# Optimization experiments

Hardware: AMD Instinct MI355X
Metric: run time of the kernel (lower is better)

The kernel has to match this reference:

```python
import jax, jax.numpy as jnp
import numpy as np

B, L, C, D, H, NB, K = 8, 1024, 4, 64, 8, 2, 16  # batch, seq, conds, dim, heads, blocks, rbf centers

def _ln(x, s, b):
    m = x.mean(-1, keepdims=True)
    v = x.var(-1, keepdims=True)
    return (x - m) / jnp.sqrt(v + 1e-6) * s + b

def setup_inputs() -> dict:
    key = jax.random.key(0)
    ks = jax.random.split(key, 24)
    rn = lambda i, shape, sc=0.02: jax.random.normal(ks[i], shape, jnp.float32) * sc
    inp = {}
    inp['z'] = jax.random.normal(ks[0], (B, L), jnp.float32)
    inp['conditionals'] = jax.random.normal(ks[1], (C,), jnp.float32)
    inp['s'] = jnp.sort(jax.random.uniform(ks[2], (L,), jnp.float32))
    inp['embed'] = rn(3, (L, 2 * D - (C + 1)))  # positional id embedding table
    # input MLP([4D, D]) with gelu
    inp['Win1'] = rn(4, (2 * D, 4 * D)); inp['bin1'] = jnp.zeros((4 * D,), jnp.float32)
    inp['Win2'] = rn(5, (4 * D, D));     inp['bin2'] = jnp.zeros((D,), jnp.float32)
    # per-block (leading dim NB) transformer params
    inp['ln1_s'] = jnp.ones((NB, D), jnp.float32); inp['ln1_b'] = jnp.zeros((NB, D), jnp.float32)
    inp['ln2_s'] = jnp.ones((NB, D), jnp.float32); inp['ln2_b'] = jnp.zeros((NB, D), jnp.float32)
    inp['Wq'] = rn(6, (NB, D, 2 * D)); inp['bq'] = jnp.zeros((NB, 2 * D), jnp.float32)
    inp['Wk'] = rn(7, (NB, D, 2 * D)); inp['bk'] = jnp.zeros((NB, 2 * D), jnp.float32)
    inp['Wv'] = rn(8, (NB, D, 2 * D)); inp['bv'] = jnp.zeros((NB, 2 * D), jnp.float32)
    inp['Wo'] = rn(9, (NB, 2 * D, D)); inp['bo'] = jnp.zeros((NB, D), jnp.float32)
    # RBF-network attention bias: features exp(-(d-c)^2/(2w^2)) -> linear to H heads
    inp['rbf_c'] = jnp.tile(jnp.linspace(-1.0, 1.0, K, dtype=jnp.float32)[None], (NB, 1))
    inp['rbf_logw'] = jnp.full((NB, K), -1.0, jnp.float32)
    inp['rbf_w'] = rn(10, (NB, K, H), 0.1); inp['rbf_b'] = jnp.zeros((NB, H), jnp.float32)
    # FFN MLP([4D, D])
    inp['W1'] = rn(11, (NB, D, 4 * D)); inp['b1'] = jnp.zeros((NB, 4 * D), jnp.float32)
    inp['W2'] = rn(12, (NB, 4 * D, D)); inp['b2'] = jnp.zeros((NB, D), jnp.float32)
    # head MLP([4D, D, 1])
    inp['Wh1'] = rn(13, (D, 4 * D)); inp['bh1'] = jnp.zeros((4 * D,), jnp.float32)
    inp['Wh2'] = rn(14, (4 * D, D)); inp['bh2'] = jnp.zeros((D,), jnp.float32)
    inp['Wh3'] = rn(15, (D, 1));     inp['bh3'] = jnp.zeros((1,), jnp.float32)
    return inp

def reference(z, conditionals, s, embed, Win1, bin1, Win2, bin2,
              ln1_s, ln1_b, ln2_s, ln2_b, Wq, bq, Wk, bk, Wv, bv, Wo, bo,
              rbf_c, rbf_logw, rbf_w, rbf_b, W1, b1, W2, b2,
              Wh1, bh1, Wh2, bh2, Wh3, bh3):
    Bn, Ln = z.shape
    Cn = conditionals.shape[0]
    Hn = rbf_w.shape[-1]
    dh = Wq.shape[-1] // Hn
    scale = 1.0 / jnp.sqrt(jnp.float32(dh))
    # cond_as_feats: [z, broadcast conditionals] -> (B, L, C+1); prepend ids embedding -> (B, L, 2D)
    feats = jnp.concatenate([
        jnp.broadcast_to(embed[None], (Bn,) + embed.shape),
        z[..., None],
        jnp.broadcast_to(conditionals[None, None, :], (Bn, Ln, Cn)),
    ], axis=-1)
    x = jax.nn.gelu(feats @ Win1 + bin1) @ Win2 + bin2  # (B, L, D)
    dist = s[:, None] - s[None, :]  # (L, L) pairwise query-key coordinate diff (same per batch)
    for i in range(Wq.shape[0]):
        h = _ln(x, ln1_s[i], ln1_b[i])
        q = (h @ Wq[i] + bq[i]).reshape(Bn, Ln, Hn, dh)
        k = (h @ Wk[i] + bk[i]).reshape(Bn, Ln, Hn, dh)
        v = (h @ Wv[i] + bv[i]).reshape(Bn, Ln, Hn, dh)
        scores = jnp.einsum('bqhd,bkhd->bhqk', q, k) * scale
        # RBF-network bias on pairwise distances, per head
        phi = jnp.exp(-(dist[..., None] - rbf_c[i]) ** 2 / (2.0 * jnp.exp(rbf_logw[i]) ** 2))  # (L, L, K)
        bias = jnp.einsum('qkf,fh->hqk', phi, rbf_w[i]) + rbf_b[i][:, None, None]  # (H, L, L)
        a = jax.nn.softmax(scores + bias[None], axis=-1)
        o = jnp.einsum('bhqk,bkhd->bqhd', a, v).reshape(Bn, Ln, Hn * dh)
        x = x + o @ Wo[i] + bo[i]
        h2 = _ln(x, ln2_s[i], ln2_b[i])
        x = x + jax.nn.gelu(h2 @ W1[i] + b1[i]) @ W2[i] + b2[i]
    hh = jax.nn.gelu(x @ Wh1 + bh1)
    hh = jax.nn.gelu(hh @ Wh2 + bh2)
    return hh @ Wh3 + bh3  # f_hat: (B, L, 1)
```

## Files before the change

### kernel.cpp

```cpp
#include <hip/hip_runtime.h>
#include <hip/hip_bf16.h>

#define BB   8
#define LL   1024
#define DD   64
#define D2   128
#define D4   256
#define HH   8
#define DH   16

typedef __attribute__((ext_vector_type(8))) short short8;
typedef __attribute__((ext_vector_type(4))) float floatx4;

#define LOG2E 1.4426950408889634f
#define QK_SEED -66.54214054f

#define OB_HALF 1048576
#define L_HALF  65536

#define OFF_WIN1   0
#define OFF_WIN2   65536
#define OFF_LAY0   98304
#define LAY_STRIDE 131072
#define OFF_WQ     0
#define OFF_WK     16384
#define OFF_WV     32768
#define OFF_WO     49152
#define OFF_W1     65536
#define OFF_W2     98304
#define OFF_WH1    360448
#define OFF_WH2    393216

__device__ __forceinline__ float gelu_tanh(float u) {
  float t = tanhf(0.7978845608028654f * (u + 0.044715f * u * u * u));
  return 0.5f * u * (1.0f + t);
}

__device__ __forceinline__ float wave_reduce_sum(float v) {
#pragma unroll
  for (int m = 32; m >= 1; m >>= 1) v += __shfl_xor(v, m, 64);
  return v;
}

__device__ __forceinline__ unsigned short f2bf(float x) {
  unsigned u = __float_as_uint(x);
  u += 0x7fffu + ((u >> 16) & 1u);
  return (unsigned short)(u >> 16);
}

__device__ __forceinline__ float bf2f(unsigned short x) {
  return __uint_as_float(((unsigned)x) << 16);
}

__device__ __forceinline__ void split_bf(float v, unsigned short& hi,
                                         unsigned short& lo) {
  hi = f2bf(v);
  lo = f2bf(v - bf2f(hi));
}

__device__ __forceinline__ unsigned pack_bf2(float a, float b) {
  unsigned ua = __float_as_uint(a) + 0x8000u;
  unsigned ub = __float_as_uint(b) + 0x8000u;
  return __builtin_amdgcn_perm(ub, ua, 0x07060302u);
}

template <int K, int KP>
__device__ __forceinline__ floatx4 mfma_tile(
    const unsigned short* Ah, const unsigned short* Al,
    const unsigned short* __restrict__ Bh, const unsigned short* __restrict__ Bl,
    int lq, int quad, floatx4 C) {
#pragma unroll
  for (int kk = 0; kk < K; kk += 32) {
    short8 ah = *(const short8*)(Ah + lq * KP + kk + quad * 8);
    short8 al = *(const short8*)(Al + lq * KP + kk + quad * 8);
    short8 bh = *(const short8*)(Bh + lq * K + kk + quad * 8);
    short8 bl = *(const short8*)(Bl + lq * K + kk + quad * 8);
    C = __builtin_amdgcn_mfma_f32_16x16x32_bf16(ah, bh, C, 0, 0, 0);
    C = __builtin_amdgcn_mfma_f32_16x16x32_bf16(al, bh, C, 0, 0, 0);
    C = __builtin_amdgcn_mfma_f32_16x16x32_bf16(ah, bl, C, 0, 0, 0);
  }
  return C;
}

struct PrepArgs {
  const float* src[16];
  int Kd[16], Nd[16], dst[16], elems[16];
};

__global__ __launch_bounds__(256) void k_prep_bias(
    PrepArgs a, unsigned short* __restrict__ arena,
    const float* __restrict__ s, const float* __restrict__ rbf_c,
    const float* __restrict__ rbf_logw, const float* __restrict__ rbf_w,
    const float* __restrict__ rbf_b, unsigned short* __restrict__ biasT) {
  int bid = blockIdx.x, t = threadIdx.x;
  if (bid < 2048) {
    int mid = bid >> 7;
    int e = (bid & 127) * 256 + t;
    int KN = a.elems[mid];
    if (e >= KN) return;
    int K = a.Kd[mid], N = a.Nd[mid];
    int n = e / K, k = e - n * K;
    float wv = a.src[mid][k * N + n];
    unsigned short hi, lo;
    split_bf(wv, hi, lo);
    arena[a.dst[mid] + e] = hi;
    arena[a.dst[mid] + KN + e] = lo;
    return;
  }
  int rem = bid - 2048;
  int lay = rem >> 12;
  int id = (rem & 4095) * 256 + t;
  int q = id >> 10, k = id & 1023;
  float dd = s[q] - s[k];
  float acc[8];
#pragma unroll
  for (int h = 0; h < 8; ++h) acc[h] = rbf_b[lay * 8 + h];
#pragma unroll 1
  for (int f = 0; f < 16; ++f) {
    float c = rbf_c[lay * 16 + f];
    float inv2w2 = 0.5f * __expf(-2.0f * rbf_logw[lay * 16 + f]);
    float e = dd - c;
    float ph = __expf(-e * e * inv2w2);
#pragma unroll
    for (int h = 0; h < 8; ++h)
      acc[h] = fmaf(ph, rbf_w[lay * 128 + f * 8 + h], acc[h]);
  }
  unsigned short* bT = biasT + (size_t)lay * 8 * 1024 * 1024;
#pragma unroll
  for (int h = 0; h < 8; ++h)
    bT[(size_t)(h * 1024 + q) * 1024 + k] = f2bf(acc[h] * LOG2E);
}

__device__ __forceinline__ void qkv_tail(
    const float* xl, unsigned short* Sh, unsigned short* Sl,
    const unsigned short* __restrict__ arena, int lay,
    const float* __restrict__ ln_s, const float* __restrict__ ln_b,
    const float* __restrict__ bq, const float* __restrict__ bk,
    const float* __restrict__ bv, unsigned short* __restrict__ qo,
    unsigned short* __restrict__ ko, unsigned short* __restrict__ voT,
    int tok0, int t) {
  int w = t >> 6, lane = t & 63;
  int lq = lane & 15, quad = lane >> 4;
  float ss = ln_s[lay * 64 + lane], sb = ln_b[lay * 64 + lane];
#pragma unroll
  for (int tk = 0; tk < 4; ++tk) {
    int tok = w * 4 + tk;
    float v = xl[tok * 64 + lane];
    float mean = wave_reduce_sum(v) * 0.015625f;
    float d = v - mean;
    float var = wave_reduce_sum(d * d) * 0.015625f;
    float hv = d * rsqrtf(var + 1e-6f) * ss + sb;
    unsigned short hi, lo;
    split_bf(hv, hi, lo);
    Sh[tok * 72 + lane] = hi;
    Sl[tok * 72 + lane] = lo;
  }
  __syncthreads();
  int b = tok0 >> 10, l0 = tok0 & 1023;
#pragma unroll 1
  for (int mat = 0; mat < 3; ++mat) {
    const unsigned short* Bh =
        arena + OFF_LAY0 + lay * LAY_STRIDE + mat * 16384;
    const unsigned short* Bl = Bh + 8192;
    const float* bias = (mat == 0 ? bq : mat == 1 ? bk : bv) + lay * 128;
#pragma unroll
    for (int j = 0; j < 2; ++j) {
      int tl = w + j * 4;
      int n = tl * 16 + lq;
      float bb = bias[n];
      floatx4 C = {bb, bb, bb, bb};
      C = mfma_tile<64, 72>(Sh, Sl, Bh + tl * 16 * 64, Bl + tl * 16 * 64,
                            lq, quad, C);
      if (mat < 2) {
        unsigned short* outp = (mat == 0 ? qo : ko);
        size_t basea = ((size_t)(b * 8 + tl) * 1024 + l0 + quad * 4) * 16 + lq;
#pragma unroll
        for (int r = 0; r < 4; ++r)
          outp[basea + (size_t)r * 16] = f2bf(C[r]);
      } else {
        size_t basev = ((size_t)(b * 8 + tl) * 16 + lq) * 1024 + l0 + quad * 4;
#pragma unroll
        for (int r = 0; r < 4; ++r)
          voT[basev + r] = f2bf(C[r]);
      }
    }
  }
}

__global__ __launch_bounds__(256) void k_in_qkv(
    const float* __restrict__ embed, const float* __restrict__ z,
    const float* __restrict__ cond, const unsigned short* __restrict__ arena,
    const float* __restrict__ bin1, const float* __restrict__ bin2,
    float* __restrict__ x, const float* __restrict__ ln1_s,
    const float* __restrict__ ln1_b, const float* __restrict__ bq,
    const float* __restrict__ bk, const float* __restrict__ bv,
    unsigned short* __restrict__ qo, unsigned short* __restrict__ ko,
    unsigned short* __restrict__ voT) {
  __shared__ __align__(16) unsigned short Ah[16 * 136], Al[16 * 136];
  __shared__ __align__(16) unsigned short Hh[16 * 264], Hl[16 * 264];
  __shared__ __align__(16) unsigned short Sh[16 * 72], Sl[16 * 72];
  __shared__ float xl[16 * 64];
  int t = threadIdx.x, w = t >> 6, lane = t & 63;
  int lq = lane & 15, quad = lane >> 4;
  int tok0 = blockIdx.x * 16;
  for (int idx = t; idx < 2048; idx += 256) {
    int tok = idx >> 7, dim = idx & 127;
    int bl = tok0 + tok, l = bl & (LL - 1);
    float v;
    if (dim < 123) v = embed[l * 123 + dim];
    else if (dim == 123) v = z[bl];
    else v = cond[dim - 124];
    unsigned short hi, lo;
    split_bf(v, hi, lo);
    Ah[tok * 136 + dim] = hi;
    Al[tok * 136 + dim] = lo;
  }
  __syncthreads();
  const unsigned short* B1h = arena + OFF_WIN1;
  const unsigned short* B1l = B1h + 32768;
#pragma unroll
  for (int j = 0; j < 4; ++j) {
    int tl = w * 4 + j, n = tl * 16 + lq;
    float bb = bin1[n];
    floatx4 C = {bb, bb, bb, bb};
    C = mfma_tile<128, 136>(Ah, Al, B1h + tl * 16 * 128, B1l + tl * 16 * 128,
                            lq, quad, C);
#pragma unroll
    for (int r = 0; r < 4; ++r) {
      float g = gelu_tanh(C[r]);
      unsigned short hi, lo;
      split_bf(g, hi, lo);
      Hh[(quad * 4 + r) * 264 + n] = hi;
      Hl[(quad * 4 + r) * 264 + n] = lo;
    }
  }
  __syncthreads();
  const unsigned short* B2h = arena + OFF_WIN2;
  const unsigned short* B2l = B2h + 16384;
  {
    int n = w * 16 + lq;
    float bb = bin2[n];
    floatx4 C = {bb, bb, bb, bb};
    C = mfma_tile<256, 264>(Hh, Hl, B2h + w * 16 * 256, B2l + w * 16 * 256,
                            lq, quad, C);
#pragma unroll
    for (int r = 0; r < 4; ++r) {
      int m = quad * 4 + r;
      x[(size_t)(tok0 + m) * 64 + n] = C[r];
      xl[m * 64 + n] = C[r];
    }
  }
  __syncthreads();
  qkv_tail(xl, Sh, Sl, arena, 0, ln1_s, ln1_b, bq, bk, bv,
           qo, ko, voT, tok0, t);
}

__global__ __launch_bounds__(256) void k_attn(
    const unsigned short* __restrict__ qg, const unsigned short* __restrict__ kg,
    const unsigned short* __restrict__ vgT, const unsigned short* __restrict__ biasT,
    float* __restrict__ og, float* __restrict__ lsum) {
  __shared__ __align__(16) unsigned short Kl[64 * 32];
  __shared__ __align__(16) unsigned short VT[16 * 72];
  __shared__ __align__(16) unsigned short Pl[4][16 * 72];
  __shared__ __align__(16) unsigned short Bch[64 * 72];
  int t = threadIdx.x, w = t >> 6, lane = t & 63;
  int lq = lane & 15, quad = lane >> 4;
  int bid = blockIdx.x;
  int half = bid >> 10;
  int rem = bid & 1023;
  int b = rem >> 7, h = (rem >> 4) & 7, qblk = rem & 15;
  int q0w = qblk * 64 + w * 16;
  int kbase = half * 512;
  size_t bh = (size_t)(b * 8 + h) * 1024;
  size_t bh16 = (size_t)(b * 8 + h) * 16;

  ((uint4*)Kl)[t] = uint4{0, 0, 0, 0};

  short8 Qb = {};
  if (quad < 2)
    Qb = *(const short8*)(qg + (bh + q0w + lq) * 16 + quad * 8);

  float l = 0.0f;
  floatx4 O = {0.0f, 0.0f, 0.0f, 0.0f};

  int key = t >> 2, dp = (t & 3) * 4;
  int drow = t >> 4, vcol = (t & 15) * 4;
  int qrow = t >> 2, bcol = (t & 3) * 16;
  const unsigned short* kgp = kg + (bh + kbase + key) * 16 + dp;
  const unsigned short* vgp = vgT + (bh16 + drow) * 1024 + kbase + vcol;
  const unsigned short* bgp =
      biasT + ((size_t)(h * 1024 + qblk * 64 + qrow)) * 1024 + kbase + bcol;

  uint2 kpre = *(const uint2*)(kgp);
  uint2 vpre = *(const uint2*)(vgp);
  uint4 bpre0 = *(const uint4*)(bgp);
  uint4 bpre1 = *(const uint4*)(bgp + 8);

#pragma unroll 1
  for (int kc = 0; kc < 512; kc += 64) {
    __syncthreads();
    *(uint2*)(Kl + key * 32 + dp) = kpre;
    *(uint2*)(VT + drow * 72 + vcol) = vpre;
    *(uint4*)(Bch + qrow * 72 + bcol) = bpre0;
    *(uint4*)(Bch + qrow * 72 + bcol + 8) = bpre1;
    __syncthreads();
    if (kc + 64 < 512) {
      kpre = *(const uint2*)(kgp + (size_t)(kc + 64) * 16);
      vpre = *(const uint2*)(vgp + (kc + 64));
      bpre0 = *(const uint4*)(bgp + (kc + 64));
      bpre1 = *(const uint4*)(bgp + (kc + 64) + 8);
    }
    float psum = 0.0f;
    unsigned short* pw = &Pl[w][lq * 72];
#pragma unroll
    for (int tile = 0; tile < 4; ++tile) {
      short8 A = *(const short8*)(Kl + (tile * 16 + lq) * 32 + quad * 8);
      floatx4 c = {QK_SEED, QK_SEED, QK_SEED, QK_SEED};
      c = __builtin_amdgcn_mfma_f32_16x16x32_bf16(A, Qb, c, 0, 0, 0);
      ushort4 bb = *(const ushort4*)(Bch + (w * 16 + lq) * 72 +
                                     tile * 16 + quad * 4);
      float p0 = exp2f(fmaf(c[0], 0.25f * LOG2E, bf2f(bb.x)));
      float p1 = exp2f(fmaf(c[1], 0.25f * LOG2E, bf2f(bb.y)));
      float p2 = exp2f(fmaf(c[2], 0.25f * LOG2E, bf2f(bb.z)));
      float p3 = exp2f(fmaf(c[3], 0.25f * LOG2E, bf2f(bb.w)));
      psum += (p0 + p1) + (p2 + p3);
      uint2 pk;
      pk.x = pack_bf2(p0, p1);
      pk.y = pack_bf2(p2, p3);
      *(uint2*)(pw + tile * 16 + quad * 4) = pk;
    }
    psum += __shfl_xor(psum, 16, 64);
    psum += __shfl_xor(psum, 32, 64);
    l += psum;
    asm volatile("s_waitcnt lgkmcnt(0)" ::: "memory");
#pragma unroll
    for (int i = 0; i < 2; ++i) {
      short8 Pa = *(const short8*)(pw + i * 32 + quad * 8);
      short8 Vb = *(const short8*)(&VT[lq * 72 + i * 32 + quad * 8]);
      O = __builtin_amdgcn_mfma_f32_16x16x32_bf16(Pa, Vb, O, 0, 0, 0);
    }
  }
  float* ogh = og + (size_t)half * OB_HALF;
#pragma unroll
  for (int r = 0; r < 4; ++r)
    ogh[((size_t)(b * 1024 + q0w + quad * 4 + r)) * 128 + h * 16 + lq] = O[r];
  if (quad == 0)
    lsum[(size_t)half * L_HALF + (size_t)(b * 1024 + q0w + lq) * 8 + h] = l;
}

__device__ __forceinline__ void pf_body(
    const float* __restrict__ ob, const float* __restrict__ lsum,
    const unsigned short* __restrict__ arena,
    const float* __restrict__ bo, float* __restrict__ x,
    const float* __restrict__ ln_s, const float* __restrict__ ln_b,
    const float* __restrict__ b1, const float* __restrict__ b2, int lay,
    unsigned short* Ah, unsigned short* Al, unsigned short* Sh,
    unsigned short* Sl, unsigned short* Hh, unsigned short* Hl, float* xl,
    int tok0, int t, bool write_x) {
  int w = t >> 6, lane = t & 63;
  int lq = lane & 15, quad = lane >> 4;
  const unsigned short* labase = arena + OFF_LAY0 + lay * LAY_STRIDE;
  const float* ob1 = ob + OB_HALF;
  for (int idx = t * 4; idx < 2048; idx += 1024) {
    int row = idx >> 7, col = idx & 127;
    int hh = col >> 4;
    int tok = tok0 + row;
    float lv = lsum[(size_t)tok * 8 + hh] +
               lsum[L_HALF + (size_t)tok * 8 + hh];
    float linv = 1.0f / lv;
    float4 v0 = *(const float4*)(ob + (size_t)tok * 128 + col);
    float4 v1 = *(const float4*)(ob1 + (size_t)tok * 128 + col);
    float4 v;
    v.x = (v0.x + v1.x) * linv;
    v.y = (v0.y + v1.y) * linv;
    v.z = (v0.z + v1.z) * linv;
    v.w = (v0.w + v1.w) * linv;
    unsigned short h0, e0, h1, e1, h2, e2, h3, e3;
    split_bf(v.x, h0, e0); split_bf(v.y, h1, e1);
    split_bf(v.z, h2, e2); split_bf(v.w, h3, e3);
    unsigned* ph = (unsigned*)(Ah + row * 136 + col);
    ph[0] = (unsigned)h0 | ((unsigned)h1 << 16);
    ph[1] = (unsigned)h2 | ((unsigned)h3 << 16);
    unsigned* pl = (unsigned*)(Al + row * 136 + col);
    pl[0] = (unsigned)e0 | ((unsigned)e1 << 16);
    pl[1] = (unsigned)e2 | ((unsigned)e3 << 16);
  }
  __syncthreads();
  {
    const unsigned short* Bh = labase + OFF_WO;
    const unsigned short* Bl = Bh + 8192;
    int n = w * 16 + lq;
    float bb = bo[lay * 64 + n];
    floatx4 C = {bb, bb, bb, bb};
    C = mfma_tile<128, 136>(Ah, Al, Bh + w * 16 * 128, Bl + w * 16 * 128,
                            lq, quad, C);
#pragma unroll
    for (int r = 0; r < 4; ++r) {
      int m = quad * 4 + r;
      xl[m * 64 + n] = x[(size_t)(tok0 + m) * 64 + n] + C[r];
    }
  }
  __syncthreads();
  {
    float ss = ln_s[lay * 64 + lane], sb = ln_b[lay * 64 + lane];
#pragma unroll
    for (int tk = 0; tk < 4; ++tk) {
      int tok = w * 4 + tk;
      float v = xl[tok * 64 + lane];
      float mean = wave_reduce_sum(v) * 0.015625f;
      float d = v - mean;
      float var = wave_reduce_sum(d * d) * 0.015625f;
      float hv = d * rsqrtf(var + 1e-6f) * ss + sb;
      unsigned short hi, lo;
      split_bf(hv, hi, lo);
      Sh[tok * 72 + lane] = hi;
      Sl[tok * 72 + lane] = lo;
    }
  }
  __syncthreads();
  {
    const unsigned short* Bh = labase + OFF_W1;
    const unsigned short* Bl = Bh + 16384;
#pragma unroll
    for (int j = 0; j < 4; ++j) {
      int tl = w * 4 + j, n = tl * 16 + lq;
      float bb = b1[lay * 256 + n];
      floatx4 C = {bb, bb, bb, bb};
      C = mfma_tile<64, 72>(Sh, Sl, Bh + tl * 16 * 64, Bl + tl * 16 * 64,
                            lq, quad, C);
#pragma unroll
      for (int r = 0; r < 4; ++r) {
        float g = gelu_tanh(C[r]);
        unsigned short hi, lo;
        split_bf(g, hi, lo);
        Hh[(quad * 4 + r) * 264 + n] = hi;
        Hl[(quad * 4 + r) * 264 + n] = lo;
      }
    }
  }
  __syncthreads();
  {
    const unsigned short* Bh = labase + OFF_W2;
    const unsigned short* Bl = Bh + 16384;
    int n = w * 16 + lq;
    float bb = b2[lay * 64 + n];
    floatx4 C = {bb, bb, bb, bb};
    C = mfma_tile<256, 264>(Hh, Hl, Bh + w * 16 * 256, Bl + w * 16 * 256,
                            lq, quad, C);
#pragma unroll
    for (int r = 0; r < 4; ++r) {
      int m = quad * 4 + r;
      float xv = xl[m * 64 + n] + C[r];
      xl[m * 64 + n] = xv;
      if (write_x) x[(size_t)(tok0 + m) * 64 + n] = xv;
    }
  }
  __syncthreads();
}

__global__ __launch_bounds__(256) void k_pf_qkv(
    const float* __restrict__ ob, const float* __restrict__ lsum,
    const unsigned short* __restrict__ arena,
    const float* __restrict__ bo, float* __restrict__ x,
    const float* __restrict__ ln2_s, const float* __restrict__ ln2_b,
    const float* __restrict__ b1, const float* __restrict__ b2, int lay,
    const float* __restrict__ ln1_s, const float* __restrict__ ln1_b,
    const float* __restrict__ bq, const float* __restrict__ bk,
    const float* __restrict__ bv, unsigned short* __restrict__ qo,
    unsigned short* __restrict__ ko, unsigned short* __restrict__ voT) {
  __shared__ __align__(16) unsigned short Ah[16 * 136], Al[16 * 136];
  __shared__ __align__(16) unsigned short Sh[16 * 72], Sl[16 * 72];
  __shared__ __align__(16) unsigned short Hh[16 * 264], Hl[16 * 264];
  __shared__ float xl[16 * 64];
  int t = threadIdx.x;
  int tok0 = blockIdx.x * 16;
  pf_body(ob, lsum, arena, bo, x, ln2_s, ln2_b, b1, b2, lay,
          Ah, Al, Sh, Sl, Hh, Hl, xl, tok0, t, true);
  qkv_tail(xl, Sh, Sl, arena, lay + 1, ln1_s, ln1_b, bq, bk, bv,
           qo, ko, voT, tok0, t);
}

__global__ __launch_bounds__(256) void k_pf_head(
    const float* __restrict__ ob, const float* __restrict__ lsum,
    const unsigned short* __restrict__ arena,
    const float* __restrict__ bo, float* __restrict__ x,
    const float* __restrict__ ln2_s, const float* __restrict__ ln2_b,
    const float* __restrict__ b1, const float* __restrict__ b2, int lay,
    const float* __restrict__ bh1, const float* __restrict__ bh2,
    const float* __restrict__ Wh3, const float* __restrict__ bh3,
    float* __restrict__ out) {
  __shared__ __align__(16) unsigned short Ah[16 * 136], Al[16 * 136];
  __shared__ __align__(16) unsigned short Sh[16 * 72], Sl[16 * 72];
  __shared__ __align__(16) unsigned short Hh[16 * 264], Hl[16 * 264];
  __shared__ float xl[16 * 64];
  int t = threadIdx.x, w = t >> 6, lane = t & 63;
  int lq = lane & 15, quad = lane >> 4;
  int tok0 = blockIdx.x * 16;
  pf_body(ob, lsum, arena, bo, x, ln2_s, ln2_b, b1, b2, lay,
          Ah, Al, Sh, Sl, Hh, Hl, xl, tok0, t, false);
#pragma unroll
  for (int tk = 0; tk < 4; ++tk) {
    int tok = w * 4 + tk;
    unsigned short hi, lo;
    split_bf(xl[tok * 64 + lane], hi, lo);
    Sh[tok * 72 + lane] = hi;
    Sl[tok * 72 + lane] = lo;
  }
  __syncthreads();
  {
    const unsigned short* Bh = arena + OFF_WH1;
    const unsigned short* Bl = Bh + 16384;
#pragma unroll
    for (int j = 0; j < 4; ++j) {
      int tl = w * 4 + j, n = tl * 16 + lq;
      float bb = bh1[n];
      floatx4 C = {bb, bb, bb, bb};
      C = mfma_tile<64, 72>(Sh, Sl, Bh + tl * 16 * 64, Bl + tl * 16 * 64,
                            lq, quad, C);
#pragma unroll
      for (int r = 0; r < 4; ++r) {
        float g = gelu_tanh(C[r]);
        unsigned short hi, lo;
        split_bf(g, hi, lo);
        Hh[(quad * 4 + r) * 264 + n] = hi;
        Hl[(quad * 4 + r) * 264 + n] = lo;
      }
    }
  }
  __syncthreads();
  {
    const unsigned short* Bh = arena + OFF_WH2;
    const unsigned short* Bl = Bh + 16384;
    int n = w * 16 + lq;
    float bb = bh2[n];
    floatx4 C = {bb, bb, bb, bb};
    C = mfma_tile<256, 264>(Hh, Hl, Bh + w * 16 * 256, Bl + w * 16 * 256,
                            lq, quad, C);
    __syncthreads();
#pragma unroll
    for (int r = 0; r < 4; ++r)
      xl[(quad * 4 + r) * 64 + n] = gelu_tanh(C[r]);
  }
  __syncthreads();
  float wv3 = Wh3[lane];
#pragma unroll
  for (int tk = 0; tk < 4; ++tk) {
    int tok = w * 4 + tk;
    float v = xl[tok * 64 + lane] * wv3;
    float sum = wave_reduce_sum(v);
    if (lane == 0) out[tok0 + tok] = sum + bh3[0];
  }
}

extern "C" void kernel_launch(void* const* d_in, const int* in_sizes, int n_in,
                              void* d_out, int out_size, void* d_ws, size_t ws_size,
                              hipStream_t stream) {
  const float* z      = (const float*)d_in[0];
  const float* cond   = (const float*)d_in[1];
  const float* s      = (const float*)d_in[2];
  const float* embed  = (const float*)d_in[3];
  const float* Win1   = (const float*)d_in[4];
  const float* bin1   = (const float*)d_in[5];
  const float* Win2   = (const float*)d_in[6];
  const float* bin2   = (const float*)d_in[7];
  const float* ln1_s  = (const float*)d_in[8];
  const float* ln1_b  = (const float*)d_in[9];
  const float* ln2_s  = (const float*)d_in[10];
  const float* ln2_b  = (const float*)d_in[11];
  const float* Wq     = (const float*)d_in[12];
  const float* bq     = (const float*)d_in[13];
  const float* Wk     = (const float*)d_in[14];
  const float* bk     = (const float*)d_in[15];
  const float* Wv     = (const float*)d_in[16];
  const float* bv     = (const float*)d_in[17];
  const float* Wo     = (const float*)d_in[18];
  const float* bo     = (const float*)d_in[19];
  const float* rbf_c  = (const float*)d_in[20];
  const float* rbf_lw = (const float*)d_in[21];
  const float* rbf_w  = (const float*)d_in[22];
  const float* rbf_b  = (const float*)d_in[23];
  const float* W1     = (const float*)d_in[24];
  const float* b1     = (const float*)d_in[25];
  const float* W2     = (const float*)d_in[26];
  const float* b2     = (const float*)d_in[27];
  const float* Wh1    = (const float*)d_in[28];
  const float* bh1    = (const float*)d_in[29];
  const float* Wh2    = (const float*)d_in[30];
  const float* bh2    = (const float*)d_in[31];
  const float* Wh3    = (const float*)d_in[32];
  const float* bh3    = (const float*)d_in[33];

  char* base = (char*)d_ws;
  float*          x     = (float*)(base);
  unsigned short* qb    = (unsigned short*)(base + (2u << 20));
  unsigned short* kb    = (unsigned short*)(base + (4u << 20));
  unsigned short* vbT   = (unsigned short*)(base + (6u << 20));
  float*          ob    = (float*)(base + (8u << 20));
  float*          lsum  = (float*)(base + (16u << 20));
  unsigned short* biasT = (unsigned short*)(base + (17u << 20));
  unsigned short* arena = (unsigned short*)(base + (50u << 20));

  PrepArgs pa;
  auto set = [&](int i, const float* sp, int K, int N, int dst) {
    pa.src[i] = sp; pa.Kd[i] = K; pa.Nd[i] = N; pa.dst[i] = dst;
    pa.elems[i] = K * N;
  };
  set(0, Win1, 128, 256, OFF_WIN1);
  set(1, Win2, 256, 64, OFF_WIN2);
  for (int lay = 0; lay < 2; ++lay) {
    int lb = OFF_LAY0 + lay * LAY_STRIDE;
    set(2 + lay * 6, Wq + lay * 8192, 64, 128, lb + OFF_WQ);
    set(3 + lay * 6, Wk + lay * 8192, 64, 128, lb + OFF_WK);
    set(4 + lay * 6, Wv + lay * 8192, 64, 128, lb + OFF_WV);
    set(5 + lay * 6, Wo + lay * 8192, 128, 64, lb + OFF_WO);
    set(6 + lay * 6, W1 + lay * 16384, 64, 256, lb + OFF_W1);
    set(7 + lay * 6, W2 + lay * 16384, 256, 64, lb + OFF_W2);
  }
  set(14, Wh1, 64, 256, OFF_WH1);
  set(15, Wh2, 256, 64, OFF_WH2);

  k_prep_bias<<<2048 + 8192, 256, 0, stream>>>(pa, arena, s, rbf_c, rbf_lw,
                                               rbf_w, rbf_b, biasT);
  k_in_qkv<<<512, 256, 0, stream>>>(embed, z, cond, arena, bin1, bin2, x,
                                    ln1_s, ln1_b, bq, bk, bv, qb, kb, vbT);
  k_attn<<<2048, 256, 0, stream>>>(qb, kb, vbT, biasT, ob, lsum);
  k_pf_qkv<<<512, 256, 0, stream>>>(ob, lsum, arena, bo, x, ln2_s, ln2_b,
                                    b1, b2, 0, ln1_s, ln1_b, bq, bk, bv,
                                    qb, kb, vbT);
  k_attn<<<2048, 256, 0, stream>>>(qb, kb, vbT,
                                   biasT + (size_t)8 * 1024 * 1024, ob, lsum);
  k_pf_head<<<512, 256, 0, stream>>>(ob, lsum, arena, bo, x, ln2_s, ln2_b,
                                     b1, b2, 1, bh1, bh2, Wh3, bh3,
                                     (float*)d_out);
}
```

Baseline: 262.1 us.

## Cheapen GELU, split MFMA accumulators, hoist RBF params, single-pass layernorm

Replaces the tanh-based GELU with an equivalent sigmoid form using fast exp and divide. Splits the three chained split-bf16 MFMAs into independent accumulators to break the dependency chain. Hoists the per-centre RBF constants into shared memory so each thread stops recomputing them. Fuses the two layernorm reductions into one pass using E[x^2]-mean^2, trading some numerical robustness for fewer shuffles.

```diff
diff --git a/kernel.cpp b/kernel.cpp
--- a/kernel.cpp
+++ b/kernel.cpp
@@ -32,8 +32,8 @@
 #define OFF_WH2    393216
 
 __device__ __forceinline__ float gelu_tanh(float u) {
-  float t = tanhf(0.7978845608028654f * (u + 0.044715f * u * u * u));
-  return 0.5f * u * (1.0f + t);
+  float y = 0.7978845608028654f * (u + 0.044715f * u * u * u);
+  return __fdividef(u, 1.0f + __expf(-2.0f * y));
 }
 
 __device__ __forceinline__ float wave_reduce_sum(float v) {
@@ -69,16 +69,20 @@
     const unsigned short* Ah, const unsigned short* Al,
     const unsigned short* __restrict__ Bh, const unsigned short* __restrict__ Bl,
     int lq, int quad, floatx4 C) {
+  floatx4 C1 = {0.0f, 0.0f, 0.0f, 0.0f};
+  floatx4 C2 = {0.0f, 0.0f, 0.0f, 0.0f};
 #pragma unroll
   for (int kk = 0; kk < K; kk += 32) {
     short8 ah = *(const short8*)(Ah + lq * KP + kk + quad * 8);
     short8 al = *(const short8*)(Al + lq * KP + kk + quad * 8);
     short8 bh = *(const short8*)(Bh + lq * K + kk + quad * 8);
     short8 bl = *(const short8*)(Bl + lq * K + kk + quad * 8);
-    C = __builtin_amdgcn_mfma_f32_16x16x32_bf16(ah, bh, C, 0, 0, 0);
-    C = __builtin_amdgcn_mfma_f32_16x16x32_bf16(al, bh, C, 0, 0, 0);
-    C = __builtin_amdgcn_mfma_f32_16x16x32_bf16(ah, bl, C, 0, 0, 0);
-  }
+    C  = __builtin_amdgcn_mfma_f32_16x16x32_bf16(ah, bh, C, 0, 0, 0);
+    C1 = __builtin_amdgcn_mfma_f32_16x16x32_bf16(al, bh, C1, 0, 0, 0);
+    C2 = __builtin_amdgcn_mfma_f32_16x16x32_bf16(ah, bl, C2, 0, 0, 0);
+  }
+#pragma unroll
+  for (int r = 0; r < 4; ++r) C[r] += C1[r] + C2[r];
   return C;
 }
 
@@ -107,8 +111,14 @@
     arena[a.dst[mid] + KN + e] = lo;
     return;
   }
+  __shared__ float cs[16], iw[16];
   int rem = bid - 2048;
   int lay = rem >> 12;
+  if (t < 16) {
+    cs[t] = rbf_c[lay * 16 + t];
+    iw[t] = 0.5f * __expf(-2.0f * rbf_logw[lay * 16 + t]);
+  }
+  __syncthreads();
   int id = (rem & 4095) * 256 + t;
   int q = id >> 10, k = id & 1023;
   float dd = s[q] - s[k];
@@ -117,10 +127,8 @@
   for (int h = 0; h < 8; ++h) acc[h] = rbf_b[lay * 8 + h];
 #pragma unroll 1
   for (int f = 0; f < 16; ++f) {
-    float c = rbf_c[lay * 16 + f];
-    float inv2w2 = 0.5f * __expf(-2.0f * rbf_logw[lay * 16 + f]);
-    float e = dd - c;
-    float ph = __expf(-e * e * inv2w2);
+    float e = dd - cs[f];
+    float ph = __expf(-e * e * iw[f]);
 #pragma unroll
     for (int h = 0; h < 8; ++h)
       acc[h] = fmaf(ph, rbf_w[lay * 128 + f * 8 + h], acc[h]);
@@ -146,10 +154,15 @@
   for (int tk = 0; tk < 4; ++tk) {
     int tok = w * 4 + tk;
     float v = xl[tok * 64 + lane];
-    float mean = wave_reduce_sum(v) * 0.015625f;
-    float d = v - mean;
-    float var = wave_reduce_sum(d * d) * 0.015625f;
-    float hv = d * rsqrtf(var + 1e-6f) * ss + sb;
+    float s1 = v, s2 = v * v;
+#pragma unroll
+    for (int m = 32; m >= 1; m >>= 1) {
+      s1 += __shfl_xor(s1, m, 64);
+      s2 += __shfl_xor(s2, m, 64);
+    }
+    float mean = s1 * 0.015625f;
+    float var = fmaf(-mean, mean, s2 * 0.015625f);
+    float hv = (v - mean) * rsqrtf(var + 1e-6f) * ss + sb;
     unsigned short hi, lo;
     split_bf(hv, hi, lo);
     Sh[tok * 72 + lane] = hi;
@@ -407,10 +420,15 @@
     for (int tk = 0; tk < 4; ++tk) {
       int tok = w * 4 + tk;
       float v = xl[tok * 64 + lane];
-      float mean = wave_reduce_sum(v) * 0.015625f;
-      float d = v - mean;
-      float var = wave_reduce_sum(d * d) * 0.015625f;
-      float hv = d * rsqrtf(var + 1e-6f) * ss + sb;
+      float s1 = v, s2 = v * v;
+#pragma unroll
+      for (int m = 32; m >= 1; m >>= 1) {
+        s1 += __shfl_xor(s1, m, 64);
+        s2 += __shfl_xor(s2, m, 64);
+      }
+      float mean = s1 * 0.015625f;
+      float var = fmaf(-mean, mean, s2 * 0.015625f);
+      float hv = (v - mean) * rsqrtf(var + 1e-6f) * ss + sb;
       unsigned short hi, lo;
       split_bf(hv, hi, lo);
       Sh[tok * 72 + lane] = hi;
```

Result: no change. 263.0 us (+0.4%).
